# Performance work log

Hardware: AMD Instinct MI355X
Metric: run time of the kernel (lower is better)

Reference implementation:

```python
import jax, jax.numpy as jnp
import numpy as np

B = 2048


def _maxpool2(x):
    return jax.lax.reduce_window(x, -jnp.inf, jax.lax.max,
                                 (1, 1, 2, 2), (1, 1, 2, 2), 'VALID')


def setup_inputs() -> dict:
    key = jax.random.key(0)
    ks = jax.random.split(key, 7)
    return {
        'x': jax.random.normal(ks[0], (B, 3, 32, 32), dtype=jnp.float32),
        'conv_w': jax.random.normal(ks[1], (45, 1, 5, 5), dtype=jnp.float32),
        'conv_b': jax.random.normal(ks[2], (45,), dtype=jnp.float32) * 0.1,
        'tree_w': jax.random.normal(ks[3], (1, 16, 15, 3, 7, 7, 2, 2), dtype=jnp.float32),
        'tree_b': jax.random.normal(ks[4], (1, 16, 3, 7), dtype=jnp.float32),
        'fc_w': jax.random.normal(ks[5], (10, 336), dtype=jnp.float32),
        'fc_b': jax.random.normal(ks[6], (10,), dtype=jnp.float32) * 0.1,
    }


def reference(x, conv_w, conv_b, tree_w, tree_b, fc_w, fc_b):
    # grouped conv: in=3, groups=3, out=45, kernel 5x5, VALID -> (B,45,28,28)
    out = jax.lax.conv_general_dilated(
        x, conv_w, window_strides=(1, 1), padding='VALID',
        dimension_numbers=('NCHW', 'OIHW', 'NCHW'), feature_group_count=3)
    out = jax.nn.sigmoid(out + conv_b[None, :, None, None])
    out = _maxpool2(out)  # (B,45,14,14)
    b = out.shape[0]
    # unfold((2,2),stride=2) + the torch reshape/transpose chain is equivalent to:
    # (B,45,14,14) -> (b, g=3, m=15, i=7, ki=2, j=7, kj=2) -> (b,m,g,i,j,ki,kj)
    xt = out.reshape(b, 3, 15, 7, 2, 7, 2).transpose(0, 2, 1, 3, 5, 4, 6)
    # TreeLayer: elementwise mul with weights (16,m,g,i,j,ki,kj) then sum over m,j,ki,kj
    t = jnp.einsum('bmgijkl,fmgijkl->bfgi', xt, tree_w[0]) + tree_b  # (B,16,3,7)
    t = jax.nn.sigmoid(t)
    return t.reshape(b, 16 * 3 * 7) @ fc_w.T + fc_b  # (B,10)
```

## Files before the change

### kernel.cpp

```cpp
#include <hip/hip_runtime.h>
#include <hip/hip_fp16.h>

#define BATCH 2048

typedef _Float16 f16x8 __attribute__((ext_vector_type(8)));
typedef float f32x4 __attribute__((ext_vector_type(4)));

__device__ __forceinline__ float fast_sigmoid(float v) {
    return __builtin_amdgcn_rcpf(1.0f + __builtin_amdgcn_exp2f(v * -1.44269504f));
}

#define WS_W3B  0
#define WS_FCW  301056

__global__ __launch_bounds__(256) void k_prep(
    const float* __restrict__ tree_w,
    const float* __restrict__ fc_w,
    ushort* __restrict__ W3B,
    float* __restrict__ FCW2,
    float* __restrict__ out)
{
    int pidx = blockIdx.x * 256 + threadIdx.x;
    if (pidx < 20480) out[pidx] = 0.f;
    if (pidx < 18816) {
        int gi = pidx / 896;
        int rem = pidx - gi * 896;
        int c = rem >> 6, lane2 = rem & 63;
        int f = lane2 & 15, qq = lane2 >> 4;
        int g = gi / 7, i = gi - g * 7;
        ushort h[8];
        #pragma unroll
        for (int u = 0; u < 8; u++) {
            int k = c * 32 + qq * 8 + u;
            int tt = k >> 6;
            int q2 = (k >> 4) & 3;
            int nn = k & 15;
            int u27 = tt * 4 + q2;
            int ki = u27 / 14;
            int pw = u27 - ki * 14;
            int j = pw >> 1, kj = pw & 1;
            float v = 0.f;
            if (nn < 15)
                v = tree_w[(size_t)f * 8820 + nn * 588 + g * 196 + i * 28
                           + j * 4 + ki * 2 + kj];
            h[u] = __half_as_ushort(__float2half(v));
        }
        *(uint4*)(W3B + (size_t)pidx * 8) = *(uint4*)h;
    } else if (pidx < 22176) {
        int j = pidx - 18816;
        int f = j & 15;
        int r = j >> 4;
        int i = r % 7;
        int r2 = r / 7;
        int o = r2 % 10;
        int g = r2 / 10;
        FCW2[j] = fc_w[o * 336 + f * 21 + g * 7 + i];
    }
}

__global__ __launch_bounds__(256, 3) void kF_all(
    const float* __restrict__ x,
    const float* __restrict__ conv_w,
    const float* __restrict__ conv_b,
    const ushort* __restrict__ W3B,
    const float* __restrict__ FCW2,
    const float* __restrict__ tree_b,
    const float* __restrict__ fc_b,
    float* __restrict__ out)
{
    __shared__ __align__(16) ushort xsc[2 * 4656];
    __shared__ __align__(16) ushort ps[4 * 3192];
    __shared__ __align__(16) ushort tsl[28 * 16];

    const int tid  = threadIdx.x;
    const int blk  = blockIdx.x;
    const int quad = blk / 3;
    const int g    = blk - quad * 3;
    const int img0 = quad * 4;
    const int lane = tid & 63;
    const int n    = lane & 15;
    const int q    = lane >> 4;
    const int wave = tid >> 6;

    float4 xv[4];
    #pragma unroll
    for (int im = 0; im < 4; im++)
        xv[im] = ((const float4*)(x + (size_t)(img0 + im) * 3072 + g * 1024))[tid];

    f16x8 B1 = {0, 0, 0, 0, 0, 0, 0, 0};
    f16x8 B2 = {0, 0, 0, 0, 0, 0, 0, 0};
    float bs = 0.f;
    if (n < 15) {
        const float* wrow = conv_w + (g * 15 + n) * 25;
        #pragma unroll
        for (int u = 0; u < 5; u++) B1[u] = (_Float16)wrow[q * 5 + u];
        if (q == 0) {
            #pragma unroll
            for (int u = 0; u < 5; u++) B2[u] = (_Float16)wrow[20 + u];
        }
        bs = conv_b[g * 15 + n] * -1.44269504f;
    }

    const int dr = (n >> 1) & 1, dc = n & 1, n4 = n >> 2;
    const int a2c = 144 - q * 36;
    int aoff[13], svr[13];
    #pragma unroll
    for (int it = 0; it < 13; it++) {
        int t = wave + it * 4;
        int pb = t * 4 + n4;
        int ph = pb / 14, pw = pb - ph * 14;
        int r = 2 * ph + dr, c = 2 * pw + dc;
        int s = c & 3;
        aoff[it] = s * 1164 + (r + q) * 36 + (c - s);
        int i = t / 7, tt = t - i * 7;
        svr[it] = i * 456 + tt * 64 + lane;
    }

    const int rowA = tid / 9, g4A = tid - rowA * 9;
    const int vB   = tid + 256;
    const int rowB = vB / 9,  g4B = vB - rowB * 9;

    auto do_shift = [&](int row, int g4) {
        #pragma unroll
        for (int im2 = 0; im2 < 2; im2++) {
            ushort* sp = xsc + im2 * 4656 + row * 36 + g4 * 4;
            if (g4 == 8) {
                uint2 z = make_uint2(0u, 0u);
                *(uint2*)(sp + 1164) = z;
                *(uint2*)(sp + 2328) = z;
                *(uint2*)(sp + 3492) = z;
            } else {
                uint2 lo = *(const uint2*)sp;
                uint2 hi = *(const uint2*)(sp + 4);
                unsigned w0 = lo.x, w1 = lo.y, w2 = hi.x, w3 = hi.y;
                unsigned t01 = (w0 >> 16) | (w1 << 16);
                unsigned t12 = (w1 >> 16) | (w2 << 16);
                unsigned t23 = (w2 >> 16) | (w3 << 16);
                *(uint2*)(sp + 1164) = make_uint2(t01, t12);
                *(uint2*)(sp + 2328) = make_uint2(w1, w2);
                *(uint2*)(sp + 3492) = make_uint2(t12, t23);
            }
        }
    };

    auto conv_tile = [&](int it, const ushort* xb, ushort* pso) {
        const ushort* pA = xb + aoff[it];
        union { struct { uint2 a, b; } u; f16x8 v; } A1, A2;
        A1.u.a = *(const uint2*)pA;
        A1.u.b = *(const uint2*)(pA + 4);
        A2.u.a = *(const uint2*)(pA + a2c);
        A2.u.b = *(const uint2*)(pA + a2c + 4);
        f32x4 d = {0.f, 0.f, 0.f, 0.f};
        d = __builtin_amdgcn_mfma_f32_16x16x32_f16(A1.v, B1, d, 0, 0, 0);
        d = __builtin_amdgcn_mfma_f32_16x16x32_f16(A2.v, B2, d, 0, 0, 0);
        float mx = fmaxf(fmaxf(d[0], d[1]), fmaxf(d[2], d[3]));
        float e = __builtin_amdgcn_exp2f(fmaf(mx, -1.44269504f, bs));
        float val = __builtin_amdgcn_rcpf(1.0f + e);
        pso[svr[it]] = __half_as_ushort(__float2half(val));
    };

    #pragma unroll
    for (int r2 = 0; r2 < 2; r2++) {
        #pragma unroll
        for (int im2 = 0; im2 < 2; im2++) {
            float4 v = xv[r2 * 2 + im2];
            int row = tid >> 3, col = (tid & 7) * 4;
            __half2 a = __float22half2_rn(make_float2(v.x, v.y));
            __half2 b = __float22half2_rn(make_float2(v.z, v.w));
            uint2 pk;
            pk.x = *(unsigned int*)&a;
            pk.y = *(unsigned int*)&b;
            *(uint2*)(xsc + im2 * 4656 + row * 36 + col) = pk;
        }
        if (tid < 64) {
            int im2 = tid >> 5, r = tid & 31;
            *(uint2*)(xsc + im2 * 4656 + r * 36 + 32) = make_uint2(0u, 0u);
        }
        __syncthreads();

        do_shift(rowA, g4A);
        if (tid < 32) do_shift(rowB, g4B);
        __syncthreads();

        #pragma unroll
        for (int im2 = 0; im2 < 2; im2++) {
            const ushort* xb = xsc + im2 * 4656;
            ushort* pso = ps + (r2 * 2 + im2) * 3192;
            #pragma unroll
            for (int it = 0; it < 12; it++) conv_tile(it, xb, pso);
            if (wave == 0) conv_tile(12, xb, pso);
        }
        __syncthreads();
    }

    for (int ii = wave; ii < 7; ii += 4) {
        const f16x8* Wb = (const f16x8*)W3B + (size_t)(g * 7 + ii) * 896;
        const ushort* ap = ps + (n & 3) * 3192 + ii * 456;
        f16x8 Bf[14];
        #pragma unroll
        for (int c = 0; c < 14; c++) Bf[c] = Wb[c * 64 + lane];
        f32x4 D0 = {0.f, 0.f, 0.f, 0.f};
        f32x4 D1 = {0.f, 0.f, 0.f, 0.f};
        #pragma unroll
        for (int c = 0; c < 7; c++) {
            f16x8 Ae = *(const f16x8*)(ap + (2 * c) * 32 + q * 8);
            D0 = __builtin_amdgcn_mfma_f32_16x16x32_f16(Ae, Bf[2 * c], D0, 0, 0, 0);
            f16x8 Ao = *(const f16x8*)(ap + (2 * c + 1) * 32 + q * 8);
            D1 = __builtin_amdgcn_mfma_f32_16x16x32_f16(Ao, Bf[2 * c + 1], D1, 0, 0, 0);
        }
        if (q == 0) {
            float tb = tree_b[n * 21 + g * 7 + ii];
            #pragma unroll
            for (int im = 0; im < 4; im++) {
                float t = (D0[im] + D1[im]) + tb;
                tsl[(im * 7 + ii) * 16 + n] =
                    __half_as_ushort(__float2half(fast_sigmoid(t)));
            }
        }
    }
    __syncthreads();

    if (lane < 10) {
        const int im4 = wave, o = lane;
        const uint2* tp = (const uint2*)(tsl + im4 * 112);
        const float4* wp = (const float4*)(FCW2 + (size_t)(g * 10 + o) * 112);
        float acc = (g == 0) ? fc_b[o] : 0.f;
        #pragma unroll
        for (int jj = 0; jj < 28; jj++) {
            float4 w4 = wp[jj];
            uint2 hv = tp[jj];
            float2 p0 = __half22float2(*(const __half2*)&hv.x);
            float2 p1 = __half22float2(*(const __half2*)&hv.y);
            acc = fmaf(p0.x, w4.x, acc);
            acc = fmaf(p0.y, w4.y, acc);
            acc = fmaf(p1.x, w4.z, acc);
            acc = fmaf(p1.y, w4.w, acc);
        }
#if defined(__HIP_PLATFORM_AMD__)
        unsafeAtomicAdd(out + (size_t)(img0 + im4) * 10 + o, acc);
#else
        atomicAdd(out + (size_t)(img0 + im4) * 10 + o, acc);
#endif
    }
}

extern "C" void kernel_launch(void* const* d_in, const int* in_sizes, int n_in,
                              void* d_out, int out_size, void* d_ws, size_t ws_size,
                              hipStream_t stream) {
    const float* x      = (const float*)d_in[0];
    const float* conv_w = (const float*)d_in[1];
    const float* conv_b = (const float*)d_in[2];
    const float* tree_w = (const float*)d_in[3];
    const float* tree_b = (const float*)d_in[4];
    const float* fc_w   = (const float*)d_in[5];
    const float* fc_b   = (const float*)d_in[6];
    float* out = (float*)d_out;

    ushort* W3B  = (ushort*)((char*)d_ws + WS_W3B);
    float*  FCW2 = (float*)((char*)d_ws + WS_FCW);

    k_prep<<<87, 256, 0, stream>>>(tree_w, fc_w, W3B, FCW2, out);
    kF_all<<<512 * 3, 256, 0, stream>>>(x, conv_w, conv_b, W3B, FCW2,
                                        tree_b, fc_b, out);
}
```

Before: 111.7 us.

## Build shifted input copies via shuffles, pair conv tiles, coalesce prep reads

The input staging now writes all four column-shifted fp16 copies of each image directly from registers, using a cross-lane shuffle for the neighbouring words. This removes the separate LDS read-and-shift pass and one barrier per round. The conv loop handles two images per call, interleaving their MFMAs to expose more independent work. LDS strides change (padding adjusted, which may shift bank conflicts). The prep kernel now reads tree_w with coalesced float4 loads and scatters fp16 writes, which needs more blocks and an extra pass that zero-fills the padding slots.

```diff
diff --git a/kernel.cpp b/kernel.cpp
--- a/kernel.cpp
+++ b/kernel.cpp
@@ -5,6 +5,12 @@
 
 typedef _Float16 f16x8 __attribute__((ext_vector_type(8)));
 typedef float f32x4 __attribute__((ext_vector_type(4)));
+
+#define RST 36
+#define CST 1168
+#define IMS 4672
+#define IST 448
+#define PIS 3152
 
 __device__ __forceinline__ float fast_sigmoid(float v) {
     return __builtin_amdgcn_rcpf(1.0f + __builtin_amdgcn_exp2f(v * -1.44269504f));
@@ -21,40 +27,48 @@
     float* __restrict__ out)
 {
     int pidx = blockIdx.x * 256 + threadIdx.x;
-    if (pidx < 20480) out[pidx] = 0.f;
-    if (pidx < 18816) {
-        int gi = pidx / 896;
-        int rem = pidx - gi * 896;
-        int c = rem >> 6, lane2 = rem & 63;
-        int f = lane2 & 15, qq = lane2 >> 4;
-        int g = gi / 7, i = gi - g * 7;
-        ushort h[8];
-        #pragma unroll
-        for (int u = 0; u < 8; u++) {
-            int k = c * 32 + qq * 8 + u;
-            int tt = k >> 6;
-            int q2 = (k >> 4) & 3;
-            int nn = k & 15;
-            int u27 = tt * 4 + q2;
-            int ki = u27 / 14;
-            int pw = u27 - ki * 14;
-            int j = pw >> 1, kj = pw & 1;
-            float v = 0.f;
-            if (nn < 15)
-                v = tree_w[(size_t)f * 8820 + nn * 588 + g * 196 + i * 28
-                           + j * 4 + ki * 2 + kj];
-            h[u] = __half_as_ushort(__float2half(v));
-        }
-        *(uint4*)(W3B + (size_t)pidx * 8) = *(uint4*)h;
-    } else if (pidx < 22176) {
-        int j = pidx - 18816;
-        int f = j & 15;
-        int r = j >> 4;
+    if (pidx < 35280) {
+        float4 v = ((const float4*)tree_w)[pidx];
+        int j  = pidx % 7;
+        int t1 = pidx / 7;
+        int i  = t1 % 7;
+        int t2 = t1 / 7;
+        int g  = t2 % 3;
+        int t3 = t2 / 3;
+        int nn = t3 % 15;
+        int f  = t3 / 15;
+        int gi = g * 7 + i;
+        int u  = nn & 7;
+        int hi = nn >> 3;
+        float vv[4] = {v.x, v.y, v.z, v.w};
+        #pragma unroll
+        for (int e = 0; e < 4; e++) {
+            int ki = e >> 1, kj = e & 1;
+            int u27 = ki * 14 + j * 2 + kj;
+            int c   = u27 >> 1;
+            int qq  = (u27 & 1) * 2 + hi;
+            W3B[(size_t)(gi * 14 + c) * 512 + (qq * 16 + f) * 8 + u] =
+                __half_as_ushort(__float2half(vv[e]));
+        }
+    } else if (pidx < 38640) {
+        int jj = pidx - 35280;
+        int f = jj & 15;
+        int r = jj >> 4;
         int i = r % 7;
         int r2 = r / 7;
         int o = r2 % 10;
         int g = r2 / 10;
-        FCW2[j] = fc_w[o * 336 + f * 21 + g * 7 + i];
+        FCW2[jj] = fc_w[o * 336 + f * 21 + g * 7 + i];
+    } else if (pidx < 48048) {
+        int z = pidx - 38640;
+        int f  = z & 15;
+        int qq = ((z >> 4) & 1) * 2 + 1;
+        int r  = z >> 5;
+        int c  = r % 14;
+        int gi = r / 14;
+        W3B[(size_t)(gi * 14 + c) * 512 + (qq * 16 + f) * 8 + 7] = 0;
+    } else if (pidx < 68528) {
+        out[pidx - 48048] = 0.f;
     }
 }
 
@@ -68,8 +82,8 @@
     const float* __restrict__ fc_b,
     float* __restrict__ out)
 {
-    __shared__ __align__(16) ushort xsc[2 * 4656];
-    __shared__ __align__(16) ushort ps[4 * 3192];
+    __shared__ __align__(16) ushort xsc[2 * IMS];
+    __shared__ __align__(16) ushort ps[4 * PIS];
     __shared__ __align__(16) ushort tsl[28 * 16];
 
     const int tid  = threadIdx.x;
@@ -102,7 +116,7 @@
     }
 
     const int dr = (n >> 1) & 1, dc = n & 1, n4 = n >> 2;
-    const int a2c = 144 - q * 36;
+    const int a2c = (4 - q) * RST;
     int aoff[13], svr[13];
     #pragma unroll
     for (int it = 0; it < 13; it++) {
@@ -111,91 +125,72 @@
         int ph = pb / 14, pw = pb - ph * 14;
         int r = 2 * ph + dr, c = 2 * pw + dc;
         int s = c & 3;
-        aoff[it] = s * 1164 + (r + q) * 36 + (c - s);
+        aoff[it] = s * CST + (r + q) * RST + (c - s);
         int i = t / 7, tt = t - i * 7;
-        svr[it] = i * 456 + tt * 64 + lane;
-    }
-
-    const int rowA = tid / 9, g4A = tid - rowA * 9;
-    const int vB   = tid + 256;
-    const int rowB = vB / 9,  g4B = vB - rowB * 9;
-
-    auto do_shift = [&](int row, int g4) {
-        #pragma unroll
-        for (int im2 = 0; im2 < 2; im2++) {
-            ushort* sp = xsc + im2 * 4656 + row * 36 + g4 * 4;
-            if (g4 == 8) {
-                uint2 z = make_uint2(0u, 0u);
-                *(uint2*)(sp + 1164) = z;
-                *(uint2*)(sp + 2328) = z;
-                *(uint2*)(sp + 3492) = z;
-            } else {
-                uint2 lo = *(const uint2*)sp;
-                uint2 hi = *(const uint2*)(sp + 4);
-                unsigned w0 = lo.x, w1 = lo.y, w2 = hi.x, w3 = hi.y;
-                unsigned t01 = (w0 >> 16) | (w1 << 16);
-                unsigned t12 = (w1 >> 16) | (w2 << 16);
-                unsigned t23 = (w2 >> 16) | (w3 << 16);
-                *(uint2*)(sp + 1164) = make_uint2(t01, t12);
-                *(uint2*)(sp + 2328) = make_uint2(w1, w2);
-                *(uint2*)(sp + 3492) = make_uint2(t12, t23);
-            }
-        }
+        svr[it] = i * IST + tt * 64 + lane;
+    }
+
+    auto conv_tile2 = [&](int it, ushort* pso) {
+        const ushort* pA0 = xsc + aoff[it];
+        const ushort* pA1 = pA0 + IMS;
+        union U { struct { uint2 a, b; } u; f16x8 v; };
+        U A1a, A2a, A1b, A2b;
+        A1a.u.a = *(const uint2*)pA0;
+        A1a.u.b = *(const uint2*)(pA0 + 4);
+        A2a.u.a = *(const uint2*)(pA0 + a2c);
+        A2a.u.b = *(const uint2*)(pA0 + a2c + 4);
+        A1b.u.a = *(const uint2*)pA1;
+        A1b.u.b = *(const uint2*)(pA1 + 4);
+        A2b.u.a = *(const uint2*)(pA1 + a2c);
+        A2b.u.b = *(const uint2*)(pA1 + a2c + 4);
+        f32x4 da = {0.f, 0.f, 0.f, 0.f}, db = {0.f, 0.f, 0.f, 0.f};
+        da = __builtin_amdgcn_mfma_f32_16x16x32_f16(A1a.v, B1, da, 0, 0, 0);
+        db = __builtin_amdgcn_mfma_f32_16x16x32_f16(A1b.v, B1, db, 0, 0, 0);
+        da = __builtin_amdgcn_mfma_f32_16x16x32_f16(A2a.v, B2, da, 0, 0, 0);
+        db = __builtin_amdgcn_mfma_f32_16x16x32_f16(A2b.v, B2, db, 0, 0, 0);
+        float mxa = fmaxf(fmaxf(da[0], da[1]), fmaxf(da[2], da[3]));
+        float mxb = fmaxf(fmaxf(db[0], db[1]), fmaxf(db[2], db[3]));
+        float ea = __builtin_amdgcn_exp2f(fmaf(mxa, -1.44269504f, bs));
+        float eb = __builtin_amdgcn_exp2f(fmaf(mxb, -1.44269504f, bs));
+        pso[svr[it]] =
+            __half_as_ushort(__float2half(__builtin_amdgcn_rcpf(1.0f + ea)));
+        pso[PIS + svr[it]] =
+            __half_as_ushort(__float2half(__builtin_amdgcn_rcpf(1.0f + eb)));
     };
 
-    auto conv_tile = [&](int it, const ushort* xb, ushort* pso) {
-        const ushort* pA = xb + aoff[it];
-        union { struct { uint2 a, b; } u; f16x8 v; } A1, A2;
-        A1.u.a = *(const uint2*)pA;
-        A1.u.b = *(const uint2*)(pA + 4);
-        A2.u.a = *(const uint2*)(pA + a2c);
-        A2.u.b = *(const uint2*)(pA + a2c + 4);
-        f32x4 d = {0.f, 0.f, 0.f, 0.f};
-        d = __builtin_amdgcn_mfma_f32_16x16x32_f16(A1.v, B1, d, 0, 0, 0);
-        d = __builtin_amdgcn_mfma_f32_16x16x32_f16(A2.v, B2, d, 0, 0, 0);
-        float mx = fmaxf(fmaxf(d[0], d[1]), fmaxf(d[2], d[3]));
-        float e = __builtin_amdgcn_exp2f(fmaf(mx, -1.44269504f, bs));
-        float val = __builtin_amdgcn_rcpf(1.0f + e);
-        pso[svr[it]] = __half_as_ushort(__float2half(val));
-    };
-
+    const int row = tid >> 3, colg = (tid & 7) * 4;
     #pragma unroll
     for (int r2 = 0; r2 < 2; r2++) {
         #pragma unroll
         for (int im2 = 0; im2 < 2; im2++) {
             float4 v = xv[r2 * 2 + im2];
-            int row = tid >> 3, col = (tid & 7) * 4;
             __half2 a = __float22half2_rn(make_float2(v.x, v.y));
             __half2 b = __float22half2_rn(make_float2(v.z, v.w));
-            uint2 pk;
-            pk.x = *(unsigned int*)&a;
-            pk.y = *(unsigned int*)&b;
-            *(uint2*)(xsc + im2 * 4656 + row * 36 + col) = pk;
-        }
-        if (tid < 64) {
-            int im2 = tid >> 5, r = tid & 31;
-            *(uint2*)(xsc + im2 * 4656 + r * 36 + 32) = make_uint2(0u, 0u);
+            unsigned d0 = *(unsigned*)&a, d1 = *(unsigned*)&b;
+            unsigned n0 = (unsigned)__shfl_down((int)d0, 1);
+            unsigned n1 = (unsigned)__shfl_down((int)d1, 1);
+            if ((tid & 7) == 7) { n0 = 0u; n1 = 0u; }
+            unsigned t01 = (d0 >> 16) | (d1 << 16);
+            unsigned t12 = (d1 >> 16) | (n0 << 16);
+            unsigned t23 = (n0 >> 16) | (n1 << 16);
+            ushort* base = xsc + im2 * IMS + row * RST + colg;
+            *(uint2*)(base)           = make_uint2(d0, d1);
+            *(uint2*)(base + CST)     = make_uint2(t01, t12);
+            *(uint2*)(base + 2 * CST) = make_uint2(d1, n0);
+            *(uint2*)(base + 3 * CST) = make_uint2(t12, t23);
         }
         __syncthreads();
 
-        do_shift(rowA, g4A);
-        if (tid < 32) do_shift(rowB, g4B);
-        __syncthreads();
-
-        #pragma unroll
-        for (int im2 = 0; im2 < 2; im2++) {
-            const ushort* xb = xsc + im2 * 4656;
-            ushort* pso = ps + (r2 * 2 + im2) * 3192;
-            #pragma unroll
-            for (int it = 0; it < 12; it++) conv_tile(it, xb, pso);
-            if (wave == 0) conv_tile(12, xb, pso);
-        }
+        ushort* pso = ps + (r2 * 2) * PIS;
+        #pragma unroll
+        for (int it = 0; it < 12; it++) conv_tile2(it, pso);
+        if (wave == 0) conv_tile2(12, pso);
         __syncthreads();
     }
 
     for (int ii = wave; ii < 7; ii += 4) {
         const f16x8* Wb = (const f16x8*)W3B + (size_t)(g * 7 + ii) * 896;
-        const ushort* ap = ps + (n & 3) * 3192 + ii * 456;
+        const ushort* ap = ps + (n & 3) * PIS + ii * IST;
         f16x8 Bf[14];
         #pragma unroll
         for (int c = 0; c < 14; c++) Bf[c] = Wb[c * 64 + lane];
@@ -259,7 +254,7 @@
     ushort* W3B  = (ushort*)((char*)d_ws + WS_W3B);
     float*  FCW2 = (float*)((char*)d_ws + WS_FCW);
 
-    k_prep<<<87, 256, 0, stream>>>(tree_w, fc_w, W3B, FCW2, out);
+    k_prep<<<268, 256, 0, stream>>>(tree_w, fc_w, W3B, FCW2, out);
     kF_all<<<512 * 3, 256, 0, stream>>>(x, conv_w, conv_b, W3B, FCW2,
                                         tree_b, fc_b, out);
 }
```

Measured after the change: 110.8 us. Within noise of the previous version (-0.8%).
